# Kernel tuning notes

Measured on AMD Instinct MI355X. Metric: run time of the kernel, lower is better.

The kernel has to match this reference:

```python
import jax, jax.numpy as jnp
import numpy as np

N, S, R, CM = 1, 128, 256, 256
C, CZ = 32, 128


def setup_inputs() -> dict:
    key = jax.random.key(0)
    k1, k2, k3, k4 = jax.random.split(key, 4)
    return {
        "msa_repr": jax.random.normal(k1, (N, S, R, CM), dtype=jnp.float32),
        "left_proj": jax.random.normal(k2, (CM, C), dtype=jnp.float32) * 0.05,
        "right_proj": jax.random.normal(k3, (CM, C), dtype=jnp.float32) * 0.05,
        "out_proj": jax.random.normal(k4, (C * C, CZ), dtype=jnp.float32) * 0.05,
    }


def reference(msa_repr, left_proj, right_proj, out_proj):
    # msa_repr: [N, S, R, CM]
    # Project to left/right activations and move R before S
    # (equivalent to torch matmul + transpose(-2, -3)).
    a = jnp.einsum("nsrm,mc->nrsc", msa_repr, left_proj)   # [N, R, S, C]
    b = jnp.einsum("nsrm,mc->nrsc", msa_repr, right_proj)  # [N, R, S, C]
    # Outer product contracted over the MSA dim S:
    # outer[n, r, t, c, e] = sum_s a[n, r, s, c] * b[n, t, s, e]
    outer = jnp.einsum("nrsc,ntse->nrtce", a, b)            # [N, R, R, C, C]
    n, r, t = outer.shape[:3]
    outer = outer.reshape(n, r, t, C * C)                   # [N, R, R, C*C]
    # Output projection to pair channels cz
    return outer @ out_proj                                 # [N, R, R, CZ]
```

## Files before the change

kernel.cpp:

```cpp
#include <hip/hip_runtime.h>

typedef __bf16 bf16x8 __attribute__((ext_vector_type(8)));
typedef __bf16 bf16x4 __attribute__((ext_vector_type(4)));
typedef float f32x16 __attribute__((ext_vector_type(16)));
typedef float f32x4 __attribute__((ext_vector_type(4)));

constexpr int S = 128, R = 256, CM = 256, C = 32, CZ = 128;

#define MFMA __builtin_amdgcn_mfma_f32_32x32x16_bf16

__device__ __forceinline__ bf16x4 cvt4(float a, float b, float c, float d) {
    bf16x4 r;
    r[0] = (__bf16)a; r[1] = (__bf16)b; r[2] = (__bf16)c; r[3] = (__bf16)d;
    return r;
}

__global__ __launch_bounds__(256) void k_wlr(const float* __restrict__ Lp,
                                             const float* __restrict__ Rp,
                                             __bf16* __restrict__ WLRT) {
    int c = blockIdx.x;
    int m = threadIdx.x;
    const float* src = (c < 32) ? Lp : Rp;
    WLRT[(size_t)c * 256 + m] = (__bf16)src[(size_t)m * 32 + (c & 31)];
}

__global__ __launch_bounds__(256) void k_projw(const float* __restrict__ msa,
                                               const __bf16* __restrict__ WLRT,
                                               const float* __restrict__ W,
                                               __bf16* __restrict__ aTf,
                                               __bf16* __restrict__ bTf,
                                               __bf16* __restrict__ WTf) {
    const int b = blockIdx.x;
    if (b >= 1024) {
        int g = (b - 1024) * 256 + threadIdx.x;
        int cz = g & 127;
        int k = g >> 7;
        int e = k >> 5, c = k & 31;
        float v = W[(size_t)(c * 32 + e) * 128 + cz];
        WTf[((size_t)(k >> 3) * 128 + cz) * 8 + (k & 7)] = (__bf16)v;
        return;
    }

    __shared__ __align__(16) __bf16 As[32 * 256];
    __shared__ __align__(16) char Pp[2 * 4096];
    const int r = b >> 2;
    const int sq = b & 3;
    const int t = threadIdx.x;

#pragma unroll
    for (int it = 0; it < 8; ++it) {
        int idx = it * 256 + t;
        int row = idx >> 6;
        int cg = idx & 63;
        float4 v = *(const float4*)&msa[((size_t)(sq * 32 + row) * R + r) * CM + cg * 4];
        bf16x4 h = cvt4(v.x, v.y, v.z, v.w);
        int P = (cg >> 1) ^ (row & 15);
        *(bf16x4*)((char*)As + row * 512 + P * 16 + (cg & 1) * 8) = h;
    }
    __syncthreads();

    const int w = t >> 6;
    const int l = t & 63;
    const int l31 = t & 31;
    const int kh = (t >> 5) & 1;
    const int sd = w & 1;
    const int ksh = w >> 1;

    f32x16 acc;
#pragma unroll
    for (int q = 0; q < 16; ++q) acc[q] = 0.f;

    const bf16x8* wb = (const bf16x8*)&WLRT[(size_t)(sd * 32 + l31) * 256 + 8 * kh];
    const char* arow = (const char*)As + l31 * 512;

    __builtin_amdgcn_s_setprio(1);
#pragma unroll
    for (int j = 0; j < 8; ++j) {
        int ks = ksh * 8 + j;
        int P = (2 * ks + kh) ^ (l31 & 15);
        bf16x8 af = *(const bf16x8*)(arow + P * 16);
        acc = MFMA(af, wb[2 * ks], acc, 0, 0, 0);
    }
    __builtin_amdgcn_s_setprio(0);

    char* pbase = Pp + (size_t)sd * 4096;
    if (ksh == 1) {
#pragma unroll
        for (int pc = 0; pc < 4; ++pc) {
            f32x4 v;
            v[0] = acc[4 * pc + 0]; v[1] = acc[4 * pc + 1];
            v[2] = acc[4 * pc + 2]; v[3] = acc[4 * pc + 3];
            *(f32x4*)(pbase + ((pc * 64) + l) * 16) = v;
        }
    }
    __syncthreads();
    if (ksh == 0) {
#pragma unroll
        for (int pc = 0; pc < 4; ++pc) {
            f32x4 v = *(const f32x4*)(pbase + ((pc * 64) + l) * 16);
            acc[4 * pc + 0] += v[0]; acc[4 * pc + 1] += v[1];
            acc[4 * pc + 2] += v[2]; acc[4 * pc + 3] += v[3];
        }
        __bf16* dst = sd ? bTf : aTf;
#pragma unroll
        for (int q = 0; q < 4; ++q) {
            size_t base = (size_t)r * 4096 + (size_t)(2 * sq + (q >> 1)) * 512 +
                          (size_t)(q & 1) * 256 + (size_t)l31 * 8 + 4 * kh;
            *(bf16x4*)&dst[base] = cvt4(acc[4 * q + 0], acc[4 * q + 1],
                                        acc[4 * q + 2], acc[4 * q + 3]);
        }
    }
}

__global__ __launch_bounds__(512, 2) void k_main(const __bf16* __restrict__ aTf,
                                                 const __bf16* __restrict__ bTf,
                                                 const __bf16* __restrict__ WTf,
                                                 float* __restrict__ out) {
    __shared__ __align__(16) __bf16 Gs[64 * 1024];

    const int t = threadIdx.x;
    const int w = t >> 6;
    const int l = t & 63;
    const int lane = l & 31;
    const int kh = l >> 5;
    const int r0 = blockIdx.x * 8;
    const int t0 = blockIdx.y * 8;

    const int rg = w & 3;
    const int tg = w >> 2;

    f32x16 acc[2][4];
#pragma unroll
    for (int i = 0; i < 2; ++i)
#pragma unroll
        for (int j = 0; j < 4; ++j)
#pragma unroll
            for (int q = 0; q < 16; ++q) acc[i][j][q] = 0.f;

    const bf16x8* ap0 = (const bf16x8*)aTf + ((size_t)(r0 + 2 * rg + 0) * 512 + kh * 32 + lane);
    const bf16x8* ap1 = (const bf16x8*)aTf + ((size_t)(r0 + 2 * rg + 1) * 512 + kh * 32 + lane);
    const bf16x8* bp0 = (const bf16x8*)bTf + ((size_t)(t0 + 4 * tg + 0) * 512 + kh * 32 + lane);
    const bf16x8* bp1 = (const bf16x8*)bTf + ((size_t)(t0 + 4 * tg + 1) * 512 + kh * 32 + lane);
    const bf16x8* bp2 = (const bf16x8*)bTf + ((size_t)(t0 + 4 * tg + 2) * 512 + kh * 32 + lane);
    const bf16x8* bp3 = (const bf16x8*)bTf + ((size_t)(t0 + 4 * tg + 3) * 512 + kh * 32 + lane);

    bf16x8 Ap[3][2], Bp[3][4];
#pragma unroll
    for (int s = 0; s < 3; ++s) {
        Ap[s][0] = ap0[s * 64]; Ap[s][1] = ap1[s * 64];
        Bp[s][0] = bp0[s * 64]; Bp[s][1] = bp1[s * 64];
        Bp[s][2] = bp2[s * 64]; Bp[s][3] = bp3[s * 64];
    }
#pragma unroll
    for (int ks = 0; ks < 8; ++ks) {
        const int s = ks % 3;
        __builtin_amdgcn_s_setprio(1);
        acc[0][0] = MFMA(Ap[s][0], Bp[s][0], acc[0][0], 0, 0, 0);
        acc[0][1] = MFMA(Ap[s][0], Bp[s][1], acc[0][1], 0, 0, 0);
        acc[0][2] = MFMA(Ap[s][0], Bp[s][2], acc[0][2], 0, 0, 0);
        acc[0][3] = MFMA(Ap[s][0], Bp[s][3], acc[0][3], 0, 0, 0);
        acc[1][0] = MFMA(Ap[s][1], Bp[s][0], acc[1][0], 0, 0, 0);
        acc[1][1] = MFMA(Ap[s][1], Bp[s][1], acc[1][1], 0, 0, 0);
        acc[1][2] = MFMA(Ap[s][1], Bp[s][2], acc[1][2], 0, 0, 0);
        acc[1][3] = MFMA(Ap[s][1], Bp[s][3], acc[1][3], 0, 0, 0);
        __builtin_amdgcn_s_setprio(0);
        if (ks + 3 < 8) {
            const int kn = ks + 3;
            Ap[s][0] = ap0[kn * 64]; Ap[s][1] = ap1[kn * 64];
            Bp[s][0] = bp0[kn * 64]; Bp[s][1] = bp1[kn * 64];
            Bp[s][2] = bp2[kn * 64]; Bp[s][3] = bp3[kn * 64];
        }
    }

    const int kq = w >> 2;
    const int ng = w & 3;
    const int czl = ng * 32 + lane;
    const char* wbc = (const char*)WTf + ((size_t)kh * 128 + czl) * 16;

    bf16x8 Wp[8];
#pragma unroll
    for (int i = 0; i < 2; ++i) {
#pragma unroll
        for (int j = 0; j < 4; ++j) {
            int p = (2 * rg + i) * 8 + 4 * tg + j;
            unsigned prow = (unsigned)p * 2048;
#pragma unroll
            for (int q = 0; q < 4; ++q) {
                int Lc = lane * 4 + q;
                int P = Lc ^ (p & 15) ^ (lane & 7);
                *(bf16x4*)((char*)Gs + prow + (unsigned)P * 16 + kh * 8) =
                    cvt4(acc[i][j][4 * q + 0], acc[i][j][4 * q + 1],
                         acc[i][j][4 * q + 2], acc[i][j][4 * q + 3]);
            }
            {
                const int u = i * 4 + j;
                asm volatile("global_load_dwordx4 %0, %1, off"
                             : "=v"(Wp[u]) : "v"(wbc + (size_t)(kq * 32 + u) * 4096));
            }
        }
    }

    asm volatile("s_waitcnt lgkmcnt(0)" ::: "memory");
    __builtin_amdgcn_s_barrier();
    __builtin_amdgcn_sched_barrier(0);

    const unsigned prow0 = (unsigned)lane * 2048;
    const unsigned prow1 = (unsigned)(lane + 32) * 2048;
    const int p15 = lane & 15;

    f32x16 o0, o1;
#pragma unroll
    for (int q = 0; q < 16; ++q) { o0[q] = 0.f; o1[q] = 0.f; }

    bf16x8 Gp[4][2];
#define LDG(sl, j) do { \
    int Lr = (kq * 32 + (j)) * 2 + kh; \
    int P = Lr ^ p15 ^ ((Lr >> 2) & 7); \
    Gp[sl][0] = *(const bf16x8*)((const char*)Gs + prow0 + (unsigned)P * 16); \
    Gp[sl][1] = *(const bf16x8*)((const char*)Gs + prow1 + (unsigned)P * 16); } while (0)

    LDG(0, 0); LDG(1, 1); LDG(2, 2); LDG(3, 3);

#define STEPB(j, cnt) do { \
    asm volatile("s_waitcnt vmcnt(" #cnt ")"); \
    __builtin_amdgcn_sched_barrier(0); \
    __builtin_amdgcn_s_setprio(1); \
    o0 = MFMA(Gp[(j) & 3][0], Wp[(j) & 7], o0, 0, 0, 0); \
    o1 = MFMA(Gp[(j) & 3][1], Wp[(j) & 7], o1, 0, 0, 0); \
    __builtin_amdgcn_s_setprio(0); \
    if ((j) + 8 < 32) { \
        asm volatile("global_load_dwordx4 %0, %1, off" \
                     : "=v"(Wp[(j) & 7]) \
                     : "v"(wbc + (size_t)(kq * 32 + (j) + 8) * 4096)); \
    } \
    if ((j) + 4 < 32) LDG((j) & 3, (j) + 4); \
} while (0)

    STEPB(0, 7);  STEPB(1, 7);  STEPB(2, 7);  STEPB(3, 7);
    STEPB(4, 7);  STEPB(5, 7);  STEPB(6, 7);  STEPB(7, 7);
    STEPB(8, 7);  STEPB(9, 7);  STEPB(10, 7); STEPB(11, 7);
    STEPB(12, 7); STEPB(13, 7); STEPB(14, 7); STEPB(15, 7);
    STEPB(16, 7); STEPB(17, 7); STEPB(18, 7); STEPB(19, 7);
    STEPB(20, 7); STEPB(21, 7); STEPB(22, 7); STEPB(23, 7);
    STEPB(24, 7); STEPB(25, 6); STEPB(26, 5); STEPB(27, 4);
    STEPB(28, 3); STEPB(29, 2); STEPB(30, 1); STEPB(31, 0);

    asm volatile("s_waitcnt lgkmcnt(0)");
    __builtin_amdgcn_s_barrier();

    if (kq == 1) {
        char* p0 = (char*)Gs + (size_t)(ng * 2 + 0) * 4096;
        char* p1 = (char*)Gs + (size_t)(ng * 2 + 1) * 4096;
#pragma unroll
        for (int pc = 0; pc < 4; ++pc) {
            f32x4 v0, v1;
            v0[0] = o0[4 * pc + 0]; v0[1] = o0[4 * pc + 1];
            v0[2] = o0[4 * pc + 2]; v0[3] = o0[4 * pc + 3];
            v1[0] = o1[4 * pc + 0]; v1[1] = o1[4 * pc + 1];
            v1[2] = o1[4 * pc + 2]; v1[3] = o1[4 * pc + 3];
            *(f32x4*)(p0 + (pc * 64 + l) * 16) = v0;
            *(f32x4*)(p1 + (pc * 64 + l) * 16) = v1;
        }
    }
    asm volatile("s_waitcnt lgkmcnt(0)");
    __builtin_amdgcn_s_barrier();

    if (kq == 0) {
        const char* p0 = (const char*)Gs + (size_t)(ng * 2 + 0) * 4096;
        const char* p1 = (const char*)Gs + (size_t)(ng * 2 + 1) * 4096;
#pragma unroll
        for (int pc = 0; pc < 4; ++pc) {
            f32x4 v0 = *(const f32x4*)(p0 + (pc * 64 + l) * 16);
            f32x4 v1 = *(const f32x4*)(p1 + (pc * 64 + l) * 16);
            o0[4 * pc + 0] += v0[0]; o0[4 * pc + 1] += v0[1];
            o0[4 * pc + 2] += v0[2]; o0[4 * pc + 3] += v0[3];
            o1[4 * pc + 0] += v1[0]; o1[4 * pc + 1] += v1[1];
            o1[4 * pc + 2] += v1[2]; o1[4 * pc + 3] += v1[3];
        }
#pragma unroll
        for (int reg = 0; reg < 16; ++reg) {
            int pl = (reg & 3) + 8 * (reg >> 2) + 4 * kh;
            int p0r = pl, p1r = 32 + pl;
            out[((size_t)(r0 + (p0r >> 3)) * 256 + (t0 + (p0r & 7))) * 128 + czl] = o0[reg];
            out[((size_t)(r0 + (p1r >> 3)) * 256 + (t0 + (p1r & 7))) * 128 + czl] = o1[reg];
        }
    }
}

extern "C" void kernel_launch(void* const* d_in, const int* in_sizes, int n_in,
                              void* d_out, int out_size, void* d_ws, size_t ws_size,
                              hipStream_t stream) {
    const float* msa = (const float*)d_in[0];
    const float* left = (const float*)d_in[1];
    const float* right = (const float*)d_in[2];
    const float* W = (const float*)d_in[3];

    __bf16* aTf = (__bf16*)d_ws;
    __bf16* bTf = aTf + (size_t)R * 4096;
    __bf16* WTf = bTf + (size_t)R * 4096;
    __bf16* WLRT = WTf + (size_t)128 * 1024;
    float* outp = (float*)d_out;

    k_wlr<<<64, 256, 0, stream>>>(left, right, WLRT);
    k_projw<<<1536, 256, 0, stream>>>(msa, WLRT, W, aTf, bTf, WTf);
    k_main<<<dim3(32, 32), 512, 0, stream>>>(aTf, bTf, WTf, outp);
}
```

Before: 58.12 us.

## Split outer-product phase into two half-width passes with explicit asm loads

Splits the first-stage outer-product MFMA loop into two passes, each covering two of the four t columns. This halves the live accumulator registers (acc[2][2] instead of acc[2][4]) and shrinks the B prefetch buffers. Loads are issued as inline asm global_load_dwordx4 with hand-placed vmcnt waits and sched_barriers, and each pass spills its results into shared memory before the next begins. The aim is lower register pressure at the two-waves-per-SIMD launch bound, at the cost of reloading the A operand twice and serialising the two passes.

```diff
diff --git a/kernel.cpp b/kernel.cpp
--- a/kernel.cpp
+++ b/kernel.cpp
@@ -128,61 +128,80 @@
 
     const int rg = w & 3;
     const int tg = w >> 2;
-
-    f32x16 acc[2][4];
-#pragma unroll
-    for (int i = 0; i < 2; ++i)
-#pragma unroll
-        for (int j = 0; j < 4; ++j)
-#pragma unroll
-            for (int q = 0; q < 16; ++q) acc[i][j][q] = 0.f;
-
-    const bf16x8* ap0 = (const bf16x8*)aTf + ((size_t)(r0 + 2 * rg + 0) * 512 + kh * 32 + lane);
-    const bf16x8* ap1 = (const bf16x8*)aTf + ((size_t)(r0 + 2 * rg + 1) * 512 + kh * 32 + lane);
-    const bf16x8* bp0 = (const bf16x8*)bTf + ((size_t)(t0 + 4 * tg + 0) * 512 + kh * 32 + lane);
-    const bf16x8* bp1 = (const bf16x8*)bTf + ((size_t)(t0 + 4 * tg + 1) * 512 + kh * 32 + lane);
-    const bf16x8* bp2 = (const bf16x8*)bTf + ((size_t)(t0 + 4 * tg + 2) * 512 + kh * 32 + lane);
-    const bf16x8* bp3 = (const bf16x8*)bTf + ((size_t)(t0 + 4 * tg + 3) * 512 + kh * 32 + lane);
-
-    bf16x8 Ap[3][2], Bp[3][4];
-#pragma unroll
-    for (int s = 0; s < 3; ++s) {
-        Ap[s][0] = ap0[s * 64]; Ap[s][1] = ap1[s * 64];
-        Bp[s][0] = bp0[s * 64]; Bp[s][1] = bp1[s * 64];
-        Bp[s][2] = bp2[s * 64]; Bp[s][3] = bp3[s * 64];
-    }
-#pragma unroll
-    for (int ks = 0; ks < 8; ++ks) {
-        const int s = ks % 3;
-        __builtin_amdgcn_s_setprio(1);
-        acc[0][0] = MFMA(Ap[s][0], Bp[s][0], acc[0][0], 0, 0, 0);
-        acc[0][1] = MFMA(Ap[s][0], Bp[s][1], acc[0][1], 0, 0, 0);
-        acc[0][2] = MFMA(Ap[s][0], Bp[s][2], acc[0][2], 0, 0, 0);
-        acc[0][3] = MFMA(Ap[s][0], Bp[s][3], acc[0][3], 0, 0, 0);
-        acc[1][0] = MFMA(Ap[s][1], Bp[s][0], acc[1][0], 0, 0, 0);
-        acc[1][1] = MFMA(Ap[s][1], Bp[s][1], acc[1][1], 0, 0, 0);
-        acc[1][2] = MFMA(Ap[s][1], Bp[s][2], acc[1][2], 0, 0, 0);
-        acc[1][3] = MFMA(Ap[s][1], Bp[s][3], acc[1][3], 0, 0, 0);
-        __builtin_amdgcn_s_setprio(0);
-        if (ks + 3 < 8) {
-            const int kn = ks + 3;
-            Ap[s][0] = ap0[kn * 64]; Ap[s][1] = ap1[kn * 64];
-            Bp[s][0] = bp0[kn * 64]; Bp[s][1] = bp1[kn * 64];
-            Bp[s][2] = bp2[kn * 64]; Bp[s][3] = bp3[kn * 64];
-        }
-    }
-
     const int kq = w >> 2;
     const int ng = w & 3;
     const int czl = ng * 32 + lane;
     const char* wbc = (const char*)WTf + ((size_t)kh * 128 + czl) * 16;
 
+    const bf16x8* ap0 = (const bf16x8*)aTf + ((size_t)(r0 + 2 * rg + 0) * 512 + kh * 32 + lane);
+    const bf16x8* ap1 = (const bf16x8*)aTf + ((size_t)(r0 + 2 * rg + 1) * 512 + kh * 32 + lane);
+    const bf16x8* bc0 = (const bf16x8*)bTf + ((size_t)(t0 + 4 * tg + 0) * 512 + kh * 32 + lane);
+    const bf16x8* bc1 = (const bf16x8*)bTf + ((size_t)(t0 + 4 * tg + 1) * 512 + kh * 32 + lane);
+    const bf16x8* bc2 = (const bf16x8*)bTf + ((size_t)(t0 + 4 * tg + 2) * 512 + kh * 32 + lane);
+    const bf16x8* bc3 = (const bf16x8*)bTf + ((size_t)(t0 + 4 * tg + 3) * 512 + kh * 32 + lane);
+
+    bf16x8 Ah[3][2], Bh[3][2];
+    f32x16 acc[2][2];
     bf16x8 Wp[8];
+
+#define ZACC() do { \
+    _Pragma("unroll") for (int i = 0; i < 2; ++i) \
+    _Pragma("unroll") for (int j = 0; j < 2; ++j) \
+    _Pragma("unroll") for (int q = 0; q < 16; ++q) acc[i][j][q] = 0.f; } while (0)
+
+#define ISSA(s, ks, B0, B1) do { \
+    asm volatile("global_load_dwordx4 %0, %1, off" : "=v"(Ah[s][0]) : "v"((const void*)(ap0 + (ks) * 64))); \
+    asm volatile("global_load_dwordx4 %0, %1, off" : "=v"(Ah[s][1]) : "v"((const void*)(ap1 + (ks) * 64))); \
+    asm volatile("global_load_dwordx4 %0, %1, off" : "=v"(Bh[s][0]) : "v"((const void*)((B0) + (ks) * 64))); \
+    asm volatile("global_load_dwordx4 %0, %1, off" : "=v"(Bh[s][1]) : "v"((const void*)((B1) + (ks) * 64))); \
+} while (0)
+
+#define STEPA(ks, cnt, B0, B1) do { \
+    asm volatile("s_waitcnt vmcnt(" #cnt ")"); \
+    __builtin_amdgcn_sched_barrier(0); \
+    __builtin_amdgcn_s_setprio(1); \
+    acc[0][0] = MFMA(Ah[(ks) % 3][0], Bh[(ks) % 3][0], acc[0][0], 0, 0, 0); \
+    acc[0][1] = MFMA(Ah[(ks) % 3][0], Bh[(ks) % 3][1], acc[0][1], 0, 0, 0); \
+    acc[1][0] = MFMA(Ah[(ks) % 3][1], Bh[(ks) % 3][0], acc[1][0], 0, 0, 0); \
+    acc[1][1] = MFMA(Ah[(ks) % 3][1], Bh[(ks) % 3][1], acc[1][1], 0, 0, 0); \
+    __builtin_amdgcn_s_setprio(0); \
+    if ((ks) + 3 < 8) ISSA((ks) % 3, (ks) + 3, B0, B1); \
+} while (0)
+
+    ZACC();
+    ISSA(0, 0, bc0, bc1); ISSA(1, 1, bc0, bc1); ISSA(2, 2, bc0, bc1);
+    STEPA(0, 8, bc0, bc1); STEPA(1, 8, bc0, bc1); STEPA(2, 8, bc0, bc1);
+    STEPA(3, 8, bc0, bc1); STEPA(4, 8, bc0, bc1); STEPA(5, 8, bc0, bc1);
+    STEPA(6, 4, bc0, bc1); STEPA(7, 0, bc0, bc1);
+
 #pragma unroll
     for (int i = 0; i < 2; ++i) {
 #pragma unroll
-        for (int j = 0; j < 4; ++j) {
+        for (int j = 0; j < 2; ++j) {
             int p = (2 * rg + i) * 8 + 4 * tg + j;
+            unsigned prow = (unsigned)p * 2048;
+#pragma unroll
+            for (int q = 0; q < 4; ++q) {
+                int Lc = lane * 4 + q;
+                int P = Lc ^ (p & 15) ^ (lane & 7);
+                *(bf16x4*)((char*)Gs + prow + (unsigned)P * 16 + kh * 8) =
+                    cvt4(acc[i][j][4 * q + 0], acc[i][j][4 * q + 1],
+                         acc[i][j][4 * q + 2], acc[i][j][4 * q + 3]);
+            }
+        }
+    }
+
+    ZACC();
+    ISSA(0, 0, bc2, bc3); ISSA(1, 1, bc2, bc3); ISSA(2, 2, bc2, bc3);
+    STEPA(0, 8, bc2, bc3); STEPA(1, 8, bc2, bc3); STEPA(2, 8, bc2, bc3);
+    STEPA(3, 8, bc2, bc3); STEPA(4, 8, bc2, bc3); STEPA(5, 8, bc2, bc3);
+    STEPA(6, 4, bc2, bc3); STEPA(7, 0, bc2, bc3);
+
+#pragma unroll
+    for (int i = 0; i < 2; ++i) {
+#pragma unroll
+        for (int j = 0; j < 2; ++j) {
+            int p = (2 * rg + i) * 8 + 4 * tg + 2 + j;
             unsigned prow = (unsigned)p * 2048;
 #pragma unroll
             for (int q = 0; q < 4; ++q) {
@@ -193,9 +212,11 @@
                          acc[i][j][4 * q + 2], acc[i][j][4 * q + 3]);
             }
             {
-                const int u = i * 4 + j;
+                const int u = i * 2 + j;
                 asm volatile("global_load_dwordx4 %0, %1, off"
-                             : "=v"(Wp[u]) : "v"(wbc + (size_t)(kq * 32 + u) * 4096));
+                             : "=v"(Wp[2 * u]) : "v"(wbc + (size_t)(kq * 32 + 2 * u) * 4096));
+                asm volatile("global_load_dwordx4 %0, %1, off"
+                             : "=v"(Wp[2 * u + 1]) : "v"(wbc + (size_t)(kq * 32 + 2 * u + 1) * 4096));
             }
         }
     }
```

Result: slower. 59.46 us (+2.3%).
